# Performance work log

Measured on AMD Instinct MI355X. Metric: run time of the kernel, lower is better.

The kernel has to match this reference:

```python
import jax, jax.numpy as jnp
import numpy as np

B, S, N = 8, 2048, 1024

def setup_inputs() -> dict:
    key = jax.random.key(0)
    k1, k2, k3 = jax.random.split(key, 3)
    outer = jax.random.normal(k1, (B, S, N), dtype=jnp.float32)
    extended_attention_mask = jnp.zeros((B, 1, S), dtype=jnp.float32)
    # torch Linear init scale ~ 1/sqrt(n)
    sc = 1.0 / np.sqrt(N)
    Wk = jax.random.normal(k2, (N, N), dtype=jnp.float32) * sc
    bk = jnp.zeros((N,), dtype=jnp.float32)
    Wq = jax.random.normal(k3, (N, N), dtype=jnp.float32) * sc
    bq = jnp.zeros((N,), dtype=jnp.float32)
    return {"outer": outer, "extended_attention_mask": extended_attention_mask,
            "Wk": Wk, "bk": bk, "Wq": Wq, "bq": bq}

def reference(outer, extended_attention_mask, Wk, bk, Wq, bq):
    # k = sigmoid(outer @ Wk^T + bk), q = sigmoid(outer @ Wq^T + bq)
    k = jax.nn.sigmoid(jnp.einsum('bsn,mn->bsm', outer, Wk) + bk)  # [B,S,N]
    q = jax.nn.sigmoid(jnp.einsum('bsn,mn->bsm', outer, Wq) + bq)  # [B,S,N]
    # scores: q @ k^T + mask -> [B,S,S]
    s = jnp.einsum('bqn,bkn->bqk', q, k) + extended_attention_mask
    attn = jax.nn.softmax(s, axis=-1)
    out = jnp.einsum('bqk,bkn->bqn', attn, outer)  # [B,S,N]
    return out.sum(-1)  # [B,S]
```

## Files before the change

### kernel.cpp

```cpp
#include <hip/hip_runtime.h>
#include <hip/hip_bf16.h>

#define BB 8
#define SS 2048
#define NN 1024
#define MT (BB*SS)
#define NPC 32
#define NG 16

typedef __attribute__((ext_vector_type(8))) short bf16x8;
typedef __attribute__((ext_vector_type(4))) float f32x4;
typedef unsigned short u16;
typedef unsigned int u32;

__device__ __forceinline__ u16 f2bf(float f) {
  u32 u = __float_as_uint(f);
  u += 0x7fff + ((u >> 16) & 1);
  return (u16)(u >> 16);
}
__device__ __forceinline__ float bf2f(u16 h) {
  return __uint_as_float(((u32)h) << 16);
}

typedef __attribute__((address_space(1))) void GV;
typedef __attribute__((address_space(3))) void LV;
__device__ __forceinline__ void cp16(const void* g, void* l) {
  __builtin_amdgcn_global_load_lds((GV*)g, (LV*)l, 16, 0, 0);
}

#define WAITV8 asm volatile("s_waitcnt vmcnt(8)" ::: "memory")
#define WAITV0 asm volatile("s_waitcnt vmcnt(0)" ::: "memory")
#define BARX   __builtin_amdgcn_s_barrier()
#define FEN    asm volatile("" ::: "memory")

__global__ __launch_bounds__(256) void prep_x_kernel(const float* __restrict__ outer,
                                                     const float* __restrict__ mask,
                                                     u16* __restrict__ Xb,
                                                     float* __restrict__ r,
                                                     float* __restrict__ kb) {
  int w = threadIdx.x >> 6, lane = threadIdx.x & 63;
  int row = blockIdx.x * 4 + w;
  const float4* src = (const float4*)(outer + (size_t)row * NN);
  ushort4* dst = (ushort4*)(Xb + (size_t)row * NN);
  float s = 0.f;
#pragma unroll
  for (int u = 0; u < 4; u++) {
    int idx = lane + u * 64;
    float4 v = src[idx];
    ushort4 o;
    o.x = f2bf(v.x); o.y = f2bf(v.y); o.z = f2bf(v.z); o.w = f2bf(v.w);
    dst[idx] = o;
    s += (v.x + v.y) + (v.z + v.w);
  }
#pragma unroll
  for (int off = 1; off < 64; off <<= 1) s += __shfl_xor(s, off);
  if (lane == 0) { r[row] = s; kb[row] = mask[row]; }
}

__global__ __launch_bounds__(256) void prep_w_kernel(const float* __restrict__ Wq,
                                                     const float* __restrict__ Wk,
                                                     const float* __restrict__ bq,
                                                     const float* __restrict__ bk,
                                                     u16* __restrict__ Wb,
                                                     float* __restrict__ bb) {
  int idx = blockIdx.x * 256 + threadIdx.x;
  int e = idx * 4;
  int rowm = e >> 10;
  int col = e & 1023;
  const float* srcp = (rowm < NN) ? (Wq + (size_t)rowm * NN + col)
                                  : (Wk + (size_t)(rowm - NN) * NN + col);
  float4 v = *(const float4*)srcp;
  ushort4 o; o.x = f2bf(v.x); o.y = f2bf(v.y); o.z = f2bf(v.z); o.w = f2bf(v.w);
  *(ushort4*)(Wb + (size_t)e) = o;
  if (idx < 2 * NN) bb[idx] = (idx < NN) ? bq[idx] : bk[idx - NN];
}

template<int LDG>
__device__ __forceinline__ void gemm_core(const u16* gA0, const u16* gB0,
                                          u16* lA, u16* lB, int tid,
                                          f32x4 (&acc)[8][4]) {
  const int row_t = tid >> 2;
  const int c8 = (tid & 3) << 3;
  const int lane = tid & 63;
  const int w = tid >> 6;
  const int wr = w >> 2, wc = w & 3;
  const int l15 = lane & 15, quad = lane >> 4;
  const u16* sA = gA0 + (size_t)row_t * LDG + c8;
  const u16* sB = gB0 + (size_t)row_t * LDG + c8;
  u16* dA = lA + row_t * 32 + c8;
  u16* dB = lB + row_t * 32 + c8;
  const u16* pa = lA + (wr * 128 + l15) * 32 + quad * 8;
  const u16* pb = lB + (wc * 64 + l15) * 32 + quad * 8;

  auto STAGE = [&](int s, int kt) {
    const u16* a_ = sA + kt * 64;
    const u16* b_ = sB + kt * 64;
    u16* la_ = dA + s * 16384;
    u16* lb_ = dB + s * 16384;
    cp16(a_, la_);                cp16(a_ + 128 * LDG, la_ + 4096);
    cp16(a_ + 32, la_ + 8192);    cp16(a_ + 32 + 128 * LDG, la_ + 12288);
    cp16(b_, lb_);                cp16(b_ + 128 * LDG, lb_ + 4096);
    cp16(b_ + 32, lb_ + 8192);    cp16(b_ + 32 + 128 * LDG, lb_ + 12288);
  };

  auto COMP = [&](int s) {
#pragma unroll
    for (int ks = 0; ks < 2; ++ks) {
      bf16x8 af[8], bf[4];
#pragma unroll
      for (int i = 0; i < 8; ++i) af[i] = *(const bf16x8*)(pa + s * 16384 + ks * 8192 + i * 512);
#pragma unroll
      for (int j = 0; j < 4; ++j) bf[j] = *(const bf16x8*)(pb + s * 16384 + ks * 8192 + j * 512);
      __builtin_amdgcn_s_setprio(1);
#pragma unroll
      for (int i = 0; i < 8; ++i)
#pragma unroll
        for (int j = 0; j < 4; ++j)
          acc[i][j] = __builtin_amdgcn_mfma_f32_16x16x32_bf16(af[i], bf[j], acc[i][j], 0, 0, 0);
      __builtin_amdgcn_s_setprio(0);
    }
  };

  STAGE(0, 0);
#pragma unroll 1
  for (int k = 0; k < NG - 2; k += 2) {
    STAGE(1, k + 1); WAITV8; BARX; FEN; COMP(0); BARX;
    STAGE(0, k + 2); WAITV8; BARX; FEN; COMP(1); BARX;
  }
  STAGE(1, NG - 1); WAITV8; BARX; FEN; COMP(0); BARX;
  WAITV0; BARX; FEN; COMP(1);
}

__global__ __launch_bounds__(512, 2) void gemm1_kernel(const u16* __restrict__ X,
                                                       const u16* __restrict__ W,
                                                       const float* __restrict__ bb,
                                                       u16* __restrict__ C,
                                                       float* __restrict__ kb) {
  __shared__ u16 lA[2 * 16384];
  __shared__ u16 lB[2 * 16384];
  int bid = blockIdx.x;
  int xcd = bid & 7, idx = bid >> 3;
  int tm = xcd * 8 + (idx & 7);
  int tn = idx >> 3;
  int tid = threadIdx.x;
  f32x4 acc[8][4] = {};
  gemm_core<1024>(X + (size_t)tm * 256 * 1024, W + (size_t)tn * 256 * 1024,
                  lA, lB, tid, acc);

  int lane = tid & 63, w = tid >> 6;
  int wr = w >> 2, wc = w & 3, l15 = lane & 15, quad = lane >> 4;
  int colb = tn * 256 + wc * 64 + l15;
  bool khalf = (tn >= 4);
  int rowb = tm * 256 + wr * 128 + quad * 4;
#pragma unroll
  for (int i = 0; i < 8; ++i) {
    float rsum[4] = {0.f, 0.f, 0.f, 0.f};
#pragma unroll
    for (int j = 0; j < 4; ++j) {
      int col = colb + j * 16;
      float bias = bb[col];
#pragma unroll
      for (int rg = 0; rg < 4; ++rg) {
        int row = rowb + i * 16 + rg;
        float v = acc[i][j][rg] + bias;
        float sg = 1.0f / (1.0f + __expf(-v));
        u16 h = f2bf(sg - 0.5f);
        C[(size_t)row * 2048 + col] = h;
        rsum[rg] += bf2f(h);
      }
    }
    if (khalf) {
#pragma unroll
      for (int rg = 0; rg < 4; ++rg) {
        float s = rsum[rg];
#pragma unroll
        for (int off = 1; off < 16; off <<= 1) s += __shfl_xor(s, off);
        if (l15 == 0) atomicAdd(&kb[rowb + i * 16 + rg], 0.5f * s);
      }
    }
  }
}

__global__ __launch_bounds__(512, 2) void flash_kernel(const u16* __restrict__ Cq,
                                                       const float* __restrict__ kb,
                                                       const float* __restrict__ r,
                                                       float* __restrict__ pm,
                                                       float* __restrict__ pl,
                                                       float* __restrict__ pt) {
  __shared__ u16 lA[2 * 16384];
  __shared__ u16 lB[2 * 16384];
  int bid = blockIdx.x;
  int b = bid & 7;
  int idx = bid >> 3;
  int qt = idx >> 3;
  int kc = idx & 7;
  int tid = threadIdx.x;
  f32x4 acc[8][4] = {};
  gemm_core<2048>(Cq + (size_t)(b * SS + qt * 256) * 2048,
                  Cq + (size_t)(b * SS + kc * 256) * 2048 + 1024,
                  lA, lB, tid, acc);

  int lane = tid & 63, w = tid >> 6;
  int wr = w >> 2, wc = w & 3, l15 = lane & 15, quad = lane >> 4;
  float kbv[4], rv[4];
  int colg = b * SS + kc * 256 + wc * 64 + l15;
#pragma unroll
  for (int j = 0; j < 4; ++j) { kbv[j] = kb[colg + j * 16]; rv[j] = r[colg + j * 16]; }
  int chunk = kc * 4 + wc;
  int rowb = b * SS + qt * 256 + wr * 128 + quad * 4;
#pragma unroll
  for (int i = 0; i < 8; ++i) {
#pragma unroll
    for (int rg = 0; rg < 4; ++rg) {
      float lg[4];
      float tmax = -1e30f;
#pragma unroll
      for (int j = 0; j < 4; ++j) { lg[j] = acc[i][j][rg] + kbv[j]; tmax = fmaxf(tmax, lg[j]); }
#pragma unroll
      for (int off = 1; off < 16; off <<= 1) tmax = fmaxf(tmax, __shfl_xor(tmax, off));
      float rs = 0.f, rt = 0.f;
#pragma unroll
      for (int j = 0; j < 4; ++j) {
        float p = __expf(lg[j] - tmax);
        rs += p; rt += p * rv[j];
      }
#pragma unroll
      for (int off = 1; off < 16; off <<= 1) { rs += __shfl_xor(rs, off); rt += __shfl_xor(rt, off); }
      if (l15 == 0) {
        int grow = rowb + i * 16 + rg;
        pm[(size_t)grow * NPC + chunk] = tmax;
        pl[(size_t)grow * NPC + chunk] = rs;
        pt[(size_t)grow * NPC + chunk] = rt;
      }
    }
  }
}

__global__ __launch_bounds__(256) void fixup_kernel(const float* __restrict__ pm,
                                                    const float* __restrict__ pl,
                                                    const float* __restrict__ pt,
                                                    float* __restrict__ out) {
  int row = blockIdx.x * 256 + threadIdx.x;
  float Mx = -1e30f;
#pragma unroll
  for (int c = 0; c < NPC; c++) Mx = fmaxf(Mx, pm[row * NPC + c]);
  float L = 0.f, T = 0.f;
#pragma unroll
  for (int c = 0; c < NPC; c++) {
    float a = __expf(pm[row * NPC + c] - Mx);
    L += pl[row * NPC + c] * a;
    T += pt[row * NPC + c] * a;
  }
  out[row] = T / L;
}

extern "C" void kernel_launch(void* const* d_in, const int* in_sizes, int n_in,
                              void* d_out, int out_size, void* d_ws, size_t ws_size,
                              hipStream_t stream) {
  const float* outer = (const float*)d_in[0];
  const float* mask  = (const float*)d_in[1];
  const float* Wk    = (const float*)d_in[2];
  const float* bk    = (const float*)d_in[3];
  const float* Wq    = (const float*)d_in[4];
  const float* bq    = (const float*)d_in[5];
  float* out = (float*)d_out;

  char* ws = (char*)d_ws;
  size_t off = 0;
  auto alloc = [&](size_t bytes) -> void* {
    void* p = ws + off;
    off = (off + bytes + 255) & ~(size_t)255;
    return p;
  };
  u16* Xb  = (u16*)alloc((size_t)MT * NN * 2);
  u16* Wb  = (u16*)alloc((size_t)2048 * NN * 2);
  u16* Cq  = (u16*)alloc((size_t)MT * 2048 * 2);
  float* bb = (float*)alloc(2048 * 4);
  float* rr = (float*)alloc((size_t)MT * 4);
  float* kb = (float*)alloc((size_t)MT * 4);
  float* pm = (float*)alloc((size_t)MT * NPC * 4);
  float* pl = (float*)alloc((size_t)MT * NPC * 4);
  float* pt = (float*)alloc((size_t)MT * NPC * 4);

  prep_x_kernel<<<dim3(MT / 4), dim3(256), 0, stream>>>(outer, mask, Xb, rr, kb);
  prep_w_kernel<<<dim3(2048), dim3(256), 0, stream>>>(Wq, Wk, bq, bk, Wb, bb);
  gemm1_kernel<<<dim3(512), dim3(512), 0, stream>>>(Xb, Wb, bb, Cq, kb);
  flash_kernel<<<dim3(512), dim3(512), 0, stream>>>(Cq, kb, rr, pm, pl, pt);
  fixup_kernel<<<dim3(MT / 256), dim3(256), 0, stream>>>(pm, pl, pt, out);
}
```

Baseline: 299.0 us.

## Restructure GEMM core into quadrant-split pipeline with swizzled LDS layout

Rewrites the shared bf16 GEMM mainloop used by both the projection GEMM and the score kernel. Global-to-LDS copies are split into per-quadrant chunks and interleaved with four MFMA sub-blocks per k-tile. An XOR swizzle on the LDS layout, 64-element rows per k-tile, is meant to cut bank conflicts. Explicit vmcnt/lgkmcnt waits and sched_barriers enforce the ordering. The aim is to overlap loads with MFMA work and shrink register fragments, at the cost of more barriers per tile and fragile hand-tuned wait counts.

```diff
diff --git a/kernel.cpp b/kernel.cpp
--- a/kernel.cpp
+++ b/kernel.cpp
@@ -6,7 +6,7 @@
 #define NN 1024
 #define MT (BB*SS)
 #define NPC 32
-#define NG 16
+#define NT 16
 
 typedef __attribute__((ext_vector_type(8))) short bf16x8;
 typedef __attribute__((ext_vector_type(4))) float f32x4;
@@ -28,10 +28,11 @@
   __builtin_amdgcn_global_load_lds((GV*)g, (LV*)l, 16, 0, 0);
 }
 
-#define WAITV8 asm volatile("s_waitcnt vmcnt(8)" ::: "memory")
-#define WAITV0 asm volatile("s_waitcnt vmcnt(0)" ::: "memory")
-#define BARX   __builtin_amdgcn_s_barrier()
-#define FEN    asm volatile("" ::: "memory")
+#define WAIT4 asm volatile("s_waitcnt vmcnt(4)" ::: "memory")
+#define WAIT6 asm volatile("s_waitcnt vmcnt(6)" ::: "memory")
+#define LGKM0 asm volatile("s_waitcnt lgkmcnt(0)" ::: "memory")
+#define BARX  __builtin_amdgcn_s_barrier()
+#define SCB0  __builtin_amdgcn_sched_barrier(0)
 
 __global__ __launch_bounds__(256) void prep_x_kernel(const float* __restrict__ outer,
                                                      const float* __restrict__ mask,
@@ -76,59 +77,89 @@
 }
 
 template<int LDG>
-__device__ __forceinline__ void gemm_core(const u16* gA0, const u16* gB0,
-                                          u16* lA, u16* lB, int tid,
+__device__ __forceinline__ void gemm_core(const u16* gA, const u16* gB,
+                                          u16* lds, int tid,
                                           f32x4 (&acc)[8][4]) {
-  const int row_t = tid >> 2;
-  const int c8 = (tid & 3) << 3;
-  const int lane = tid & 63;
-  const int w = tid >> 6;
+  const int lane = tid & 63, w = tid >> 6;
   const int wr = w >> 2, wc = w & 3;
-  const int l15 = lane & 15, quad = lane >> 4;
-  const u16* sA = gA0 + (size_t)row_t * LDG + c8;
-  const u16* sB = gB0 + (size_t)row_t * LDG + c8;
-  u16* dA = lA + row_t * 32 + c8;
-  u16* dB = lB + row_t * 32 + c8;
-  const u16* pa = lA + (wr * 128 + l15) * 32 + quad * 8;
-  const u16* pb = lB + (wc * 64 + l15) * 32 + quad * 8;
-
-  auto STAGE = [&](int s, int kt) {
-    const u16* a_ = sA + kt * 64;
-    const u16* b_ = sB + kt * 64;
-    u16* la_ = dA + s * 16384;
-    u16* lb_ = dB + s * 16384;
-    cp16(a_, la_);                cp16(a_ + 128 * LDG, la_ + 4096);
-    cp16(a_ + 32, la_ + 8192);    cp16(a_ + 32 + 128 * LDG, la_ + 12288);
-    cp16(b_, lb_);                cp16(b_ + 128 * LDG, lb_ + 4096);
-    cp16(b_ + 32, lb_ + 8192);    cp16(b_ + 32 + 128 * LDG, lb_ + 12288);
-  };
-
-  auto COMP = [&](int s) {
-#pragma unroll
-    for (int ks = 0; ks < 2; ++ks) {
-      bf16x8 af[8], bf[4];
-#pragma unroll
-      for (int i = 0; i < 8; ++i) af[i] = *(const bf16x8*)(pa + s * 16384 + ks * 8192 + i * 512);
-#pragma unroll
-      for (int j = 0; j < 4; ++j) bf[j] = *(const bf16x8*)(pb + s * 16384 + ks * 8192 + j * 512);
-      __builtin_amdgcn_s_setprio(1);
-#pragma unroll
-      for (int i = 0; i < 8; ++i)
-#pragma unroll
-        for (int j = 0; j < 4; ++j)
-          acc[i][j] = __builtin_amdgcn_mfma_f32_16x16x32_bf16(af[i], bf[j], acc[i][j], 0, 0, 0);
-      __builtin_amdgcn_s_setprio(0);
-    }
-  };
-
-  STAGE(0, 0);
+  const int l15 = lane & 15, quad = lane >> 4, xq = l15 & 7;
+  const int lr = lane >> 3, lc = lane & 7;
+  const int sslot = lc ^ lr;
+  const int so0 = ((quad ^ xq)) * 8;
+  const int so1 = (((4 + quad) ^ xq)) * 8;
+
+  const u16* gAr = gA + (size_t)(wr * 128 + wc * 8 + lr) * LDG + sslot * 8;
+  const u16* gBr = gB + (size_t)(wc * 64 + wr * 8 + lr) * LDG + sslot * 8;
+
+  auto STA = [&](int buf, int lo, int kt) {
+    cp16(gAr + (size_t)lo * 32 * LDG + kt * 64,
+         lds + buf * 32768 + wr * 8192 + ((lo * 4 + wc) * 64 + lane) * 8);
+  };
+  auto STB = [&](int buf, int lb, int kt) {
+    cp16(gBr + (size_t)lb * 16 * LDG + kt * 64,
+         lds + buf * 32768 + 16384 + wc * 4096 + ((lb * 2 + wr) * 64 + lane) * 8);
+  };
+
+  bf16x8 af[4][2], bf[2][2];
+  auto LDA4 = [&](int buf, int ih) {
+#pragma unroll
+    for (int i2 = 0; i2 < 4; ++i2) {
+      const u16* p = lds + buf * 32768 + wr * 8192 + (ih * 64 + i2 * 16 + l15) * 64;
+      af[i2][0] = *(const bf16x8*)(p + so0);
+      af[i2][1] = *(const bf16x8*)(p + so1);
+    }
+  };
+  auto LDB2 = [&](int buf, int jh) {
+#pragma unroll
+    for (int j2 = 0; j2 < 2; ++j2) {
+      const u16* p = lds + buf * 32768 + 16384 + wc * 4096 + ((jh * 2 + j2) * 16 + l15) * 64;
+      bf[j2][0] = *(const bf16x8*)(p + so0);
+      bf[j2][1] = *(const bf16x8*)(p + so1);
+    }
+  };
+  auto MQ = [&](int ih, int jh) {
+    __builtin_amdgcn_s_setprio(1);
+#pragma unroll
+    for (int ks = 0; ks < 2; ++ks)
+#pragma unroll
+      for (int i2 = 0; i2 < 4; ++i2)
+#pragma unroll
+        for (int j2 = 0; j2 < 2; ++j2)
+          acc[ih * 4 + i2][jh * 2 + j2] =
+              __builtin_amdgcn_mfma_f32_16x16x32_bf16(af[i2][ks], bf[j2][ks],
+                                                      acc[ih * 4 + i2][jh * 2 + j2], 0, 0, 0);
+    __builtin_amdgcn_s_setprio(0);
+  };
+
+  STA(0, 0, 0); STA(0, 1, 0); STB(0, 0, 0); STB(0, 1, 0);
+  STB(0, 2, 0); STB(0, 3, 0); STA(0, 2, 0); STA(0, 3, 0);
+  WAIT4; BARX;
+
 #pragma unroll 1
-  for (int k = 0; k < NG - 2; k += 2) {
-    STAGE(1, k + 1); WAITV8; BARX; FEN; COMP(0); BARX;
-    STAGE(0, k + 2); WAITV8; BARX; FEN; COMP(1); BARX;
-  }
-  STAGE(1, NG - 1); WAITV8; BARX; FEN; COMP(0); BARX;
-  WAITV0; BARX; FEN; COMP(1);
+  for (int t = 0; t < NT; ++t) {
+    const int buf = t & 1, nb = buf ^ 1, nt = t + 1;
+    const bool st = (t < NT - 1);
+    LDA4(buf, 0); LDB2(buf, 0);
+    if (st) { STA(nb, 0, nt); STA(nb, 1, nt); }
+    WAIT4; BARX; LGKM0; SCB0;
+    MQ(0, 0);
+    BARX;
+    LDB2(buf, 1);
+    if (st) { STB(nb, 0, nt); STB(nb, 1, nt); }
+    WAIT4; BARX; LGKM0; SCB0;
+    MQ(0, 1);
+    BARX;
+    LDA4(buf, 1);
+    if (st) { STB(nb, 2, nt); STB(nb, 3, nt); }
+    WAIT6; BARX; LGKM0; SCB0;
+    MQ(1, 1);
+    BARX;
+    LDB2(buf, 0);
+    if (st) { STA(nb, 2, nt); STA(nb, 3, nt); }
+    WAIT4; BARX; LGKM0; SCB0;
+    MQ(1, 0);
+    BARX;
+  }
 }
 
 __global__ __launch_bounds__(512, 2) void gemm1_kernel(const u16* __restrict__ X,
@@ -136,8 +167,7 @@
                                                        const float* __restrict__ bb,
                                                        u16* __restrict__ C,
                                                        float* __restrict__ kb) {
-  __shared__ u16 lA[2 * 16384];
-  __shared__ u16 lB[2 * 16384];
+  __shared__ u16 lds[2 * 32768];
   int bid = blockIdx.x;
   int xcd = bid & 7, idx = bid >> 3;
   int tm = xcd * 8 + (idx & 7);
@@ -145,7 +175,7 @@
   int tid = threadIdx.x;
   f32x4 acc[8][4] = {};
   gemm_core<1024>(X + (size_t)tm * 256 * 1024, W + (size_t)tn * 256 * 1024,
-                  lA, lB, tid, acc);
+                  lds, tid, acc);
 
   int lane = tid & 63, w = tid >> 6;
   int wr = w >> 2, wc = w & 3, l15 = lane & 15, quad = lane >> 4;
@@ -187,8 +217,7 @@
                                                        float* __restrict__ pm,
                                                        float* __restrict__ pl,
                                                        float* __restrict__ pt) {
-  __shared__ u16 lA[2 * 16384];
-  __shared__ u16 lB[2 * 16384];
+  __shared__ u16 lds[2 * 32768];
   int bid = blockIdx.x;
   int b = bid & 7;
   int idx = bid >> 3;
@@ -198,7 +227,7 @@
   f32x4 acc[8][4] = {};
   gemm_core<2048>(Cq + (size_t)(b * SS + qt * 256) * 2048,
                   Cq + (size_t)(b * SS + kc * 256) * 2048 + 1024,
-                  lA, lB, tid, acc);
+                  lds, tid, acc);
 
   int lane = tid & 63, w = tid >> 6;
   int wr = w >> 2, wc = w & 3, l15 = lane & 15, quad = lane >> 4;
```

Result: faster. 283.9 us (-5.1%).
